# Optimization experiments

Measured on AMD Instinct MI355X. Metric: run time of the kernel, lower is better.

Reference implementation:

```python
import jax, jax.numpy as jnp
import numpy as np

RES = 256       # image resolution (even)
N_ANGLES = 180  # projection angles over [0, pi)
BATCH = 4


def _compute_rays(resolution):
    # Same as Radon._compute_rays: vertical chords of inscribed circle.
    s = resolution // 2
    locations = np.arange(2 * s) - s + 0.5
    ys = np.sqrt(s ** 2 - locations ** 2) + 0.5
    rays = np.stack([locations, -ys, locations, ys], axis=1)  # [R,4]
    return jnp.asarray(rays, dtype=jnp.float32)


def setup_inputs() -> dict:
    key = jax.random.key(0)
    imgs = jax.random.normal(key, (BATCH, RES, RES), dtype=jnp.float32)
    angles = jnp.linspace(0.0, np.pi, N_ANGLES, endpoint=False).astype(jnp.float32)
    rays = _compute_rays(RES)
    return {"imgs": imgs, "angles": angles, "rays": rays}


def reference(imgs, angles, rays):
    # imgs: [B,res,res]; angles: [A]; rays: [R,4] -> sinogram [B,A,R]
    res = imgs.shape[-1]
    s = res // 2
    n_steps = res  # integration samples per ray (~1px spacing across the circle)

    start = rays[:, :2]   # [R,2]
    end = rays[:, 2:]     # [R,2]
    length = jnp.sqrt(jnp.sum((end - start) ** 2, axis=-1))  # [R]

    c, sn = jnp.cos(angles), jnp.sin(angles)
    # rotation matrices [A,2,2] (CCW rotation of ray endpoints)
    rot = jnp.stack([jnp.stack([c, -sn], -1), jnp.stack([sn, c], -1)], -2)
    start_r = jnp.einsum('aij,rj->ari', rot, start)  # [A,R,2]
    end_r = jnp.einsum('aij,rj->ari', rot, end)      # [A,R,2]

    t = (jnp.arange(n_steps, dtype=jnp.float32) + 0.5) / n_steps  # [T]
    # sample points along each rotated ray: [A,R,T,2]
    pts = start_r[:, :, None, :] + t[None, None, :, None] * (end_r - start_r)[:, :, None, :]

    # world (x,y) -> continuous pixel coords (pixel centers at integer coords)
    fx = pts[..., 0] + (s - 0.5)  # [A,R,T]
    fy = pts[..., 1] + (s - 0.5)
    x0 = jnp.floor(fx)
    y0 = jnp.floor(fy)
    wx = fx - x0
    wy = fy - y0
    x0i = x0.astype(jnp.int32)
    y0i = y0.astype(jnp.int32)

    def gather(ix, iy):
        # zero-padded bilinear corner fetch, batched over imgs
        valid = (ix >= 0) & (ix < res) & (iy >= 0) & (iy < res)
        ixc = jnp.clip(ix, 0, res - 1)
        iyc = jnp.clip(iy, 0, res - 1)
        vals = imgs[:, iyc, ixc]  # [B,A,R,T]
        return jnp.where(valid[None], vals, jnp.float32(0))

    v00 = gather(x0i, y0i)
    v01 = gather(x0i + 1, y0i)
    v10 = gather(x0i, y0i + 1)
    v11 = gather(x0i + 1, y0i + 1)

    samp = (v00 * ((1 - wx) * (1 - wy))[None]
            + v01 * (wx * (1 - wy))[None]
            + v10 * ((1 - wx) * wy)[None]
            + v11 * (wx * wy)[None])  # [B,A,R,T]

    # line integral: sum of samples * step length along the ray
    sino = samp.sum(-1) * (length / n_steps)[None, None, :]  # [B,A,R]
    return sino
```

## Files before the change

kernel.cpp:

```cpp
#include <hip/hip_runtime.h>

#define RES   256
#define NANG  180
#define NRAYS 256
#define NPIX  (RES * RES)
#define OUTP  (NANG * NRAYS)

#define PITCH 258
#define PADN  (PITCH * PITCH)

#define SHALLOW_BLOCKS (90 * 8)
#define STEEP_BLOCKS   (90 * 16)
#define TOTAL_BLOCKS   (SHALLOW_BLOCKS + STEEP_BLOCKS)

typedef _Float16 half2v __attribute__((ext_vector_type(2)));

__device__ __forceinline__ float hdot(unsigned int p, half2v w, float acc) {
#if __has_builtin(__builtin_amdgcn_fdot2)
    return __builtin_amdgcn_fdot2(__builtin_bit_cast(half2v, p), w, acc, false);
#else
    half2v v = __builtin_bit_cast(half2v, p);
    return acc + (float)v.x * (float)w.x + (float)v.y * (float)w.y;
#endif
}

__global__ __launch_bounds__(256) void pad_pairs(
    const float* __restrict__ imgs, uint4* __restrict__ timg)
{
    const int idx = blockIdx.x * 256 + threadIdx.x;
    if (idx >= PADN) return;
    const int y = idx / PITCH, x = idx - y * PITCH;
    const int iy = y - 1;
    const bool ry = (unsigned)iy < (unsigned)RES;
    const bool r0 = ry && ((unsigned)(x - 1) < (unsigned)RES);
    const bool r1 = ry && ((unsigned)x < (unsigned)RES);
    const int s0 = iy * RES + (x - 1);
    const int s1 = iy * RES + x;

    unsigned int u[4];
#pragma unroll
    for (int b = 0; b < 4; ++b) {
        const float v0 = r0 ? imgs[b * NPIX + s0] : 0.0f;
        const float v1 = r1 ? imgs[b * NPIX + s1] : 0.0f;
        half2v h; h.x = (_Float16)v0; h.y = (_Float16)v1;
        u[b] = __builtin_bit_cast(unsigned int, h);
    }
    timg[idx] = make_uint4(u[0], u[1], u[2], u[3]);
}

struct Geom { float srx, sry, ddx, ddy, scale; };

__device__ __forceinline__ Geom make_geom(const float* __restrict__ angles,
                                          const float* __restrict__ rays,
                                          int a, int r)
{
    float sn, cs;
    sincosf(angles[a], &sn, &cs);
    const float4 ray = reinterpret_cast<const float4*>(rays)[r];
    const float dxr = ray.z - ray.x, dyr = ray.w - ray.y;
    const float len = sqrtf(dxr * dxr + dyr * dyr);
    Geom g;
    g.srx = cs * ray.x - sn * ray.y + 127.5f;
    g.sry = sn * ray.x + cs * ray.y + 127.5f;
    g.ddx = (cs * ray.z - sn * ray.w + 127.5f) - g.srx;
    g.ddy = (sn * ray.z + cs * ray.w + 127.5f) - g.sry;
    g.scale = len * (1.0f / RES);
    return g;
}

__device__ __forceinline__ void sample8(
    const uint4* __restrict__ timg,
    float& fx, float& fy, float dfx, float dfy,
    float acc0[4], float acc1[4])
{
    uint4 r0[8], r1[8];
    float wxv[8], wyv[8];

#pragma unroll
    for (int j = 0; j < 8; ++j) {
        const float x0f = floorf(fx), y0f = floorf(fy);
        wxv[j] = fx - x0f;
        wyv[j] = fy - y0f;
        const int idx = (int)y0f * PITCH + (int)x0f + (PITCH + 1);
        r0[j] = timg[idx];
        r1[j] = timg[idx + PITCH];
        fx += dfx; fy += dfy;
    }

#pragma unroll
    for (int j = 0; j < 8; ++j) {
        const float wx = wxv[j], wy = wyv[j];
        const float w11 = wx * wy;
        const float w01 = wx - w11;
        const float w10 = wy - w11;
        const float w00 = (1.0f - wx) - w10;

        half2v wa; wa.x = (_Float16)w00; wa.y = (_Float16)w01;
        half2v wb; wb.x = (_Float16)w10; wb.y = (_Float16)w11;

        float* acc = (j & 1) ? acc1 : acc0;
        acc[0] = hdot(r0[j].x, wa, hdot(r1[j].x, wb, acc[0]));
        acc[1] = hdot(r0[j].y, wa, hdot(r1[j].y, wb, acc[1]));
        acc[2] = hdot(r0[j].z, wa, hdot(r1[j].z, wb, acc[2]));
        acc[3] = hdot(r0[j].w, wa, hdot(r1[j].w, wb, acc[3]));
    }
}

__global__ __launch_bounds__(512, 4) void radon_main(
    const uint4*  __restrict__ timg,
    const float*  __restrict__ angles,
    const float*  __restrict__ rays,
    float*        __restrict__ out)
{
    const int bid = blockIdx.x;
    const int tid = threadIdx.x;

    if (bid < SHALLOW_BLOCKS) {
        const int as = bid >> 3;
        const int rg = bid & 7;
        const int a  = (as < 45) ? as : as + 90;
        const int tx = tid & 31;
        const int ty = tid >> 5;
        const int r  = rg * 32 + tx;

        const Geom g = make_geom(angles, rays, a, r);
        float acc0[4] = {0.f, 0.f, 0.f, 0.f};
        float acc1[4] = {0.f, 0.f, 0.f, 0.f};

        const float dfx = g.ddx * (1.0f / RES);
        const float dfy = g.ddy * (1.0f / RES);
        float fx = fmaf(((float)(ty * 8) + 0.5f) * (1.0f / RES), g.ddx, g.srx);
        float fy = fmaf(((float)(ty * 8) + 0.5f) * (1.0f / RES), g.ddy, g.sry);

        sample8(timg, fx, fy, dfx, dfy, acc0, acc1);
        fx += g.ddx * (120.0f / RES);
        fy += g.ddy * (120.0f / RES);
        sample8(timg, fx, fy, dfx, dfy, acc0, acc1);

        __shared__ float red[4][16][32];
#pragma unroll
        for (int b = 0; b < 4; ++b) red[b][ty][tx] = acc0[b] + acc1[b];
        __syncthreads();

        if (tid < 128) {
            const int b  = tid >> 5;
            const int t2 = tid & 31;
            float s = 0.f;
#pragma unroll
            for (int j = 0; j < 16; ++j) s += red[b][j][t2];
            out[b * OUTP + a * NRAYS + rg * 32 + t2] = s * g.scale;
        }
    } else {
        const int b2   = bid - SHALLOW_BLOCKS;
        const int a    = (b2 >> 4) + 45;
        const int rq   = b2 & 15;
        const int w    = tid >> 6;
        const int lane = tid & 63;
        const int half = lane >> 5;
        const int sub  = lane & 31;
        const int r    = rq * 16 + w * 2 + half;

        const Geom g = make_geom(angles, rays, a, r);
        float acc0[4] = {0.f, 0.f, 0.f, 0.f};
        float acc1[4] = {0.f, 0.f, 0.f, 0.f};

        float fx = fmaf(((float)sub + 0.5f) * (1.0f / RES), g.ddx, g.srx);
        float fy = fmaf(((float)sub + 0.5f) * (1.0f / RES), g.ddy, g.sry);
        const float dfx = g.ddx * 0.125f;
        const float dfy = g.ddy * 0.125f;

        sample8(timg, fx, fy, dfx, dfy, acc0, acc1);

        float a0 = acc0[0] + acc1[0];
        float a1 = acc0[1] + acc1[1];
        float a2 = acc0[2] + acc1[2];
        float a3 = acc0[3] + acc1[3];

#pragma unroll
        for (int m = 1; m < 32; m <<= 1) {
            a0 += __shfl_xor(a0, m, 64);
            a1 += __shfl_xor(a1, m, 64);
            a2 += __shfl_xor(a2, m, 64);
            a3 += __shfl_xor(a3, m, 64);
        }
        if (sub == 0) {
            const int base = a * NRAYS + r;
            out[0 * OUTP + base] = a0 * g.scale;
            out[1 * OUTP + base] = a1 * g.scale;
            out[2 * OUTP + base] = a2 * g.scale;
            out[3 * OUTP + base] = a3 * g.scale;
        }
    }
}

__global__ __launch_bounds__(256) void radon_simple(
    const float* __restrict__ imgs,
    const float* __restrict__ angles,
    const float* __restrict__ rays,
    float* __restrict__ out)
{
    const int a = blockIdx.x;
    const int r = threadIdx.x;
    const Geom g = make_geom(angles, rays, a, r);
    float a0 = 0.f, a1 = 0.f, a2 = 0.f, a3 = 0.f;
    for (int k = 0; k < RES; ++k) {
        const float t  = ((float)k + 0.5f) * (1.0f / RES);
        const float fx = fmaf(t, g.ddx, g.srx);
        const float fy = fmaf(t, g.ddy, g.sry);
        const float x0f = floorf(fx), y0f = floorf(fy);
        const float wx = fx - x0f, wy = fy - y0f;
        const int x0 = (int)x0f, y0 = (int)y0f;
        const bool vx0 = (unsigned)x0 < (unsigned)RES;
        const bool vx1 = (unsigned)(x0 + 1) < (unsigned)RES;
        const bool vy0 = (unsigned)y0 < (unsigned)RES;
        const bool vy1 = (unsigned)(y0 + 1) < (unsigned)RES;
        const int x0c = min(max(x0, 0), RES - 1), x1c = min(max(x0 + 1, 0), RES - 1);
        const int y0c = min(max(y0, 0), RES - 1), y1c = min(max(y0 + 1, 0), RES - 1);
        const float omwx = 1.0f - wx, omwy = 1.0f - wy;
        const float w00 = (vx0 && vy0) ? omwx * omwy : 0.f;
        const float w01 = (vx1 && vy0) ? wx * omwy : 0.f;
        const float w10 = (vx0 && vy1) ? omwx * wy : 0.f;
        const float w11 = (vx1 && vy1) ? wx * wy : 0.f;
        const int i00 = y0c * RES + x0c, i01 = y0c * RES + x1c;
        const int i10 = y1c * RES + x0c, i11 = y1c * RES + x1c;
        a0 = fmaf(w00, imgs[i00], fmaf(w01, imgs[i01], fmaf(w10, imgs[i10], fmaf(w11, imgs[i11], a0))));
        a1 = fmaf(w00, imgs[NPIX + i00], fmaf(w01, imgs[NPIX + i01], fmaf(w10, imgs[NPIX + i10], fmaf(w11, imgs[NPIX + i11], a1))));
        a2 = fmaf(w00, imgs[2 * NPIX + i00], fmaf(w01, imgs[2 * NPIX + i01], fmaf(w10, imgs[2 * NPIX + i10], fmaf(w11, imgs[2 * NPIX + i11], a2))));
        a3 = fmaf(w00, imgs[3 * NPIX + i00], fmaf(w01, imgs[3 * NPIX + i01], fmaf(w10, imgs[3 * NPIX + i10], fmaf(w11, imgs[3 * NPIX + i11], a3))));
    }
    const int base = a * NRAYS + r;
    out[0 * OUTP + base] = a0 * g.scale;
    out[1 * OUTP + base] = a1 * g.scale;
    out[2 * OUTP + base] = a2 * g.scale;
    out[3 * OUTP + base] = a3 * g.scale;
}

extern "C" void kernel_launch(void* const* d_in, const int* in_sizes, int n_in,
                              void* d_out, int out_size, void* d_ws, size_t ws_size,
                              hipStream_t stream) {
    const float* imgs   = (const float*)d_in[0];
    const float* angles = (const float*)d_in[1];
    const float* rays   = (const float*)d_in[2];
    float* out = (float*)d_out;

    const size_t need = (size_t)PADN * sizeof(uint4);

    if (ws_size >= need) {
        uint4* timg = (uint4*)d_ws;
        pad_pairs<<<(PADN + 255) / 256, 256, 0, stream>>>(imgs, timg);
        radon_main<<<TOTAL_BLOCKS, 512, 0, stream>>>(timg, angles, rays, out);
    } else {
        radon_simple<<<NANG, NRAYS, 0, stream>>>(imgs, angles, rays, out);
    }
}
```

Baseline: 34.60 us.

## Add transposed padded image so steep rays sample along contiguous memory

The pad kernel now builds a second padded fp16 pair image that is transposed. Steep-angle rays sample this copy with their x and y coordinates swapped, so each step moves mostly along a row instead of across rows. The aim is fewer cache lines per sample and better locality for the steep-ray blocks, which are the larger share of the work. In exchange, the preprocessing kernel doubles its writes and does strided, uncoalesced reads for the transposed copy, and the workspace requirement doubles. `sample8` now takes its coordinates by value, so the shallow path's second-half offset changes from 120 to 128 steps to keep the same sample positions.

```diff
diff --git a/kernel.cpp b/kernel.cpp
--- a/kernel.cpp
+++ b/kernel.cpp
@@ -25,27 +25,48 @@
 }
 
 __global__ __launch_bounds__(256) void pad_pairs(
-    const float* __restrict__ imgs, uint4* __restrict__ timg)
+    const float* __restrict__ imgs,
+    uint4* __restrict__ timgX, uint4* __restrict__ timgT)
 {
     const int idx = blockIdx.x * 256 + threadIdx.x;
     if (idx >= PADN) return;
-    const int y = idx / PITCH, x = idx - y * PITCH;
-    const int iy = y - 1;
-    const bool ry = (unsigned)iy < (unsigned)RES;
-    const bool r0 = ry && ((unsigned)(x - 1) < (unsigned)RES);
-    const bool r1 = ry && ((unsigned)x < (unsigned)RES);
-    const int s0 = iy * RES + (x - 1);
-    const int s1 = iy * RES + x;
-
-    unsigned int u[4];
-#pragma unroll
-    for (int b = 0; b < 4; ++b) {
-        const float v0 = r0 ? imgs[b * NPIX + s0] : 0.0f;
-        const float v1 = r1 ? imgs[b * NPIX + s1] : 0.0f;
-        half2v h; h.x = (_Float16)v0; h.y = (_Float16)v1;
-        u[b] = __builtin_bit_cast(unsigned int, h);
-    }
-    timg[idx] = make_uint4(u[0], u[1], u[2], u[3]);
+    const int p = idx / PITCH, q = idx - p * PITCH;
+
+    {
+        const int iy = p - 1;
+        const bool ry = (unsigned)iy < (unsigned)RES;
+        const bool c0 = ry && ((unsigned)(q - 1) < (unsigned)RES);
+        const bool c1 = ry && ((unsigned)q < (unsigned)RES);
+        const int s0 = iy * RES + (q - 1);
+        const int s1 = iy * RES + q;
+        unsigned int u[4];
+#pragma unroll
+        for (int b = 0; b < 4; ++b) {
+            const float v0 = c0 ? imgs[b * NPIX + s0] : 0.0f;
+            const float v1 = c1 ? imgs[b * NPIX + s1] : 0.0f;
+            half2v h; h.x = (_Float16)v0; h.y = (_Float16)v1;
+            u[b] = __builtin_bit_cast(unsigned int, h);
+        }
+        timgX[idx] = make_uint4(u[0], u[1], u[2], u[3]);
+    }
+
+    {
+        const int ix = p - 1;
+        const bool rx = (unsigned)ix < (unsigned)RES;
+        const bool c0 = rx && ((unsigned)(q - 1) < (unsigned)RES);
+        const bool c1 = rx && ((unsigned)q < (unsigned)RES);
+        const int s0 = (q - 1) * RES + ix;
+        const int s1 = q * RES + ix;
+        unsigned int u[4];
+#pragma unroll
+        for (int b = 0; b < 4; ++b) {
+            const float v0 = c0 ? imgs[b * NPIX + s0] : 0.0f;
+            const float v1 = c1 ? imgs[b * NPIX + s1] : 0.0f;
+            half2v h; h.x = (_Float16)v0; h.y = (_Float16)v1;
+            u[b] = __builtin_bit_cast(unsigned int, h);
+        }
+        timgT[idx] = make_uint4(u[0], u[1], u[2], u[3]);
+    }
 }
 
 struct Geom { float srx, sry, ddx, ddy, scale; };
@@ -70,30 +91,30 @@
 
 __device__ __forceinline__ void sample8(
     const uint4* __restrict__ timg,
-    float& fx, float& fy, float dfx, float dfy,
+    float fA, float fB, float dA, float dB,
     float acc0[4], float acc1[4])
 {
     uint4 r0[8], r1[8];
-    float wxv[8], wyv[8];
+    float wAv[8], wBv[8];
 
 #pragma unroll
     for (int j = 0; j < 8; ++j) {
-        const float x0f = floorf(fx), y0f = floorf(fy);
-        wxv[j] = fx - x0f;
-        wyv[j] = fy - y0f;
-        const int idx = (int)y0f * PITCH + (int)x0f + (PITCH + 1);
+        const float A0 = floorf(fA), B0 = floorf(fB);
+        wAv[j] = fA - A0;
+        wBv[j] = fB - B0;
+        const int idx = (int)B0 * PITCH + (int)A0 + (PITCH + 1);
         r0[j] = timg[idx];
         r1[j] = timg[idx + PITCH];
-        fx += dfx; fy += dfy;
+        fA += dA; fB += dB;
     }
 
 #pragma unroll
     for (int j = 0; j < 8; ++j) {
-        const float wx = wxv[j], wy = wyv[j];
-        const float w11 = wx * wy;
-        const float w01 = wx - w11;
-        const float w10 = wy - w11;
-        const float w00 = (1.0f - wx) - w10;
+        const float wA = wAv[j], wB = wBv[j];
+        const float w11 = wA * wB;
+        const float w01 = wA - w11;
+        const float w10 = wB - w11;
+        const float w00 = (1.0f - wA) - w10;
 
         half2v wa; wa.x = (_Float16)w00; wa.y = (_Float16)w01;
         half2v wb; wb.x = (_Float16)w10; wb.y = (_Float16)w11;
@@ -107,7 +128,8 @@
 }
 
 __global__ __launch_bounds__(512, 4) void radon_main(
-    const uint4*  __restrict__ timg,
+    const uint4*  __restrict__ timgX,
+    const uint4*  __restrict__ timgT,
     const float*  __restrict__ angles,
     const float*  __restrict__ rays,
     float*        __restrict__ out)
@@ -132,10 +154,10 @@
         float fx = fmaf(((float)(ty * 8) + 0.5f) * (1.0f / RES), g.ddx, g.srx);
         float fy = fmaf(((float)(ty * 8) + 0.5f) * (1.0f / RES), g.ddy, g.sry);
 
-        sample8(timg, fx, fy, dfx, dfy, acc0, acc1);
-        fx += g.ddx * (120.0f / RES);
-        fy += g.ddy * (120.0f / RES);
-        sample8(timg, fx, fy, dfx, dfy, acc0, acc1);
+        sample8(timgX, fx, fy, dfx, dfy, acc0, acc1);
+        fx += g.ddx * (128.0f / RES);
+        fy += g.ddy * (128.0f / RES);
+        sample8(timgX, fx, fy, dfx, dfy, acc0, acc1);
 
         __shared__ float red[4][16][32];
 #pragma unroll
@@ -169,7 +191,7 @@
         const float dfx = g.ddx * 0.125f;
         const float dfy = g.ddy * 0.125f;
 
-        sample8(timg, fx, fy, dfx, dfy, acc0, acc1);
+        sample8(timgT, fy, fx, dfy, dfx, acc0, acc1);
 
         float a0 = acc0[0] + acc1[0];
         float a1 = acc0[1] + acc1[1];
@@ -243,12 +265,13 @@
     const float* rays   = (const float*)d_in[2];
     float* out = (float*)d_out;
 
-    const size_t need = (size_t)PADN * sizeof(uint4);
-
-    if (ws_size >= need) {
-        uint4* timg = (uint4*)d_ws;
-        pad_pairs<<<(PADN + 255) / 256, 256, 0, stream>>>(imgs, timg);
-        radon_main<<<TOTAL_BLOCKS, 512, 0, stream>>>(timg, angles, rays, out);
+    const size_t one = (size_t)PADN * sizeof(uint4);
+
+    if (ws_size >= 2 * one) {
+        uint4* timgX = (uint4*)d_ws;
+        uint4* timgT = (uint4*)((char*)d_ws + one);
+        pad_pairs<<<(PADN + 255) / 256, 256, 0, stream>>>(imgs, timgX, timgT);
+        radon_main<<<TOTAL_BLOCKS, 512, 0, stream>>>(timgX, timgT, angles, rays, out);
     } else {
         radon_simple<<<NANG, NRAYS, 0, stream>>>(imgs, angles, rays, out);
     }
```

Result: slower. 39.07 us (+12.9%).
